# Kernel optimization log

Hardware: AMD Instinct MI355X
Metric: run time of the kernel (lower is better)

The kernel has to match this reference:

```python
import jax, jax.numpy as jnp
import numpy as np

N_CLIENTS = 1_000_000
N_ITEMS = 100_000
D = 128          # embedding_dim (in_feats)
H = 128          # output_size (h_feats)
N_NODES = 100_000
N_EDGES = 1_600_000


def setup_inputs() -> dict:
    key = jax.random.key(0)
    ks = jax.random.split(key, 12)
    f32 = jnp.float32
    return {
        # TwoPartEmbedding tables
        "client_table": jax.random.normal(ks[0], (N_CLIENTS, D), dtype=f32) * 0.02,
        "item_table": jax.random.normal(ks[1], (N_ITEMS, D), dtype=f32) * 0.02,
        # SAGEConv layer 1 (in_feats -> h_feats)
        "W_self1": jax.random.normal(ks[2], (D, H), dtype=f32) * (1.0 / np.sqrt(D)),
        "W_neigh1": jax.random.normal(ks[3], (D, H), dtype=f32) * (1.0 / np.sqrt(D)),
        "b1": jnp.zeros((H,), dtype=f32),
        # SAGEConv layer 2 (h_feats -> h_feats)
        "W_self2": jax.random.normal(ks[4], (H, H), dtype=f32) * (1.0 / np.sqrt(H)),
        "W_neigh2": jax.random.normal(ks[5], (H, H), dtype=f32) * (1.0 / np.sqrt(H)),
        "b2": jnp.zeros((H,), dtype=f32),
        # subgraph data
        "node_ids": jax.random.randint(ks[6], (N_NODES,), 0, N_CLIENTS + N_ITEMS),
        "src": jax.random.randint(ks[7], (N_EDGES,), 0, N_NODES),
        "dst": jax.random.randint(ks[8], (N_EDGES,), 0, N_NODES),
    }


def _two_part_embedding(node_ids, client_table, item_table):
    # IDs < N_CLIENTS index the client table; the rest (offset) index the item table.
    is_client = node_ids < N_CLIENTS
    cx = client_table[jnp.where(is_client, node_ids, 0)]              # [N, D]
    ix = item_table[jnp.where(is_client, 0, node_ids - N_CLIENTS)]    # [N, D]
    return jnp.where(is_client[:, None], cx, ix)


def _sage_layer(x, src, dst, W_self, W_neigh, b):
    # DGL SAGEConv, mean aggregator: gather src features, segment-mean onto dst.
    msg = x[src]  # [E, d]
    agg = jax.ops.segment_sum(msg, dst, num_segments=N_NODES)
    deg = jax.ops.segment_sum(jnp.ones((src.shape[0],), dtype=x.dtype), dst,
                              num_segments=N_NODES)
    h_neigh = agg / jnp.maximum(deg, 1.0)[:, None]
    return x @ W_self + h_neigh @ W_neigh + b


def reference(client_table, item_table, W_self1, W_neigh1, b1,
              W_self2, W_neigh2, b2, node_ids, src, dst):
    x = _two_part_embedding(node_ids, client_table, item_table)       # [N, D]
    h = jax.nn.relu(_sage_layer(x, src, dst, W_self1, W_neigh1, b1))  # [N, H]
    out = _sage_layer(h, src, dst, W_self2, W_neigh2, b2)             # [N, H]
    return out
```

## Files before the change

### kernel.cpp

```cpp
#include <hip/hip_runtime.h>


#define N_CLIENTS 1000000
#define N_NODES   100000
#define N_EDGES   1600000
#define DCAP      64

typedef unsigned short u16;
typedef unsigned int   u32;
typedef __bf16  bf16x8 __attribute__((ext_vector_type(8)));
typedef float   f32x4  __attribute__((ext_vector_type(4)));

__device__ __forceinline__ u16 f2bf(float f) {
    union { float f; u32 i; } c; c.f = f;
    u32 r = c.i + 0x7FFFu + ((c.i >> 16) & 1u);
    return (u16)(r >> 16);
}
__device__ __forceinline__ float2 bfpair(u32 u) {
    union { u32 i; float f; } lo, hi;
    lo.i = u << 16; hi.i = u & 0xFFFF0000u;
    return make_float2(lo.f, hi.f);
}

__global__ __launch_bounds__(256) void prep_kernel(
    const float* __restrict__ W0, const float* __restrict__ W1,
    const float* __restrict__ W2, const float* __restrict__ W3,
    u16* __restrict__ Wt)
{
    int i = blockIdx.x * 256 + threadIdx.x;
    int mat = i >> 14, k = (i >> 7) & 127, n = i & 127;
    const float* W = mat == 0 ? W0 : mat == 1 ? W1 : mat == 2 ? W2 : W3;
    Wt[mat * 16384 + n * 128 + k] = f2bf(W[k * 128 + n]);
}

__global__ __launch_bounds__(256) void embed_kernel(
    const float* __restrict__ client, const float* __restrict__ item,
    const int* __restrict__ ids, u16* __restrict__ Xb)
{
    int t = blockIdx.x * 256 + threadIdx.x;
    int node = t >> 5, j = t & 31;
    if (node >= N_NODES) return;
    int id = ids[node];
    const float4* row = (id < N_CLIENTS)
        ? (const float4*)(client + (size_t)id * 128)
        : (const float4*)(item + (size_t)(id - N_CLIENTS) * 128);
    float4 v = row[j];
    uint2 o;
    o.x = ((u32)f2bf(v.y) << 16) | f2bf(v.x);
    o.y = ((u32)f2bf(v.w) << 16) | f2bf(v.z);
    *(uint2*)(Xb + (size_t)node * 128 + j * 4) = o;
}

__global__ __launch_bounds__(256) void scatter_kernel(
    const int* __restrict__ src, const int* __restrict__ dst,
    int* __restrict__ cnt, int* __restrict__ bucket)
{
    int e = blockIdx.x * 256 + threadIdx.x;
    if (e >= N_EDGES) return;
    int d = dst[e];
    int pos = atomicAdd(&cnt[d], 1);
    if (pos < DCAP) bucket[(size_t)d * DCAP + pos] = src[e];
}

__global__ __launch_bounds__(256) void agg_kernel(
    const u16* __restrict__ Xb, const int* __restrict__ cnt,
    const int* __restrict__ bucket, u16* __restrict__ HNb)
{
    int wid = (blockIdx.x * 256 + threadIdx.x) >> 6;
    wid = __builtin_amdgcn_readfirstlane(wid);
    int lane = threadIdx.x & 63;
    if (wid >= N_NODES) return;
    int d = cnt[wid];
    int dc = d < DCAP ? d : DCAP;
    const int* bk = bucket + (size_t)wid * DCAP;
    float ax = 0.f, ay = 0.f;
    int e = 0;
    for (; e + 4 <= dc; e += 4) {
        int s0 = bk[e+0], s1 = bk[e+1], s2 = bk[e+2], s3 = bk[e+3];
        u32 u0 = *(const u32*)(Xb + (size_t)s0 * 128 + lane * 2);
        u32 u1 = *(const u32*)(Xb + (size_t)s1 * 128 + lane * 2);
        u32 u2 = *(const u32*)(Xb + (size_t)s2 * 128 + lane * 2);
        u32 u3 = *(const u32*)(Xb + (size_t)s3 * 128 + lane * 2);
        float2 v0 = bfpair(u0), v1 = bfpair(u1), v2 = bfpair(u2), v3 = bfpair(u3);
        ax += v0.x + v1.x + v2.x + v3.x;
        ay += v0.y + v1.y + v2.y + v3.y;
    }
    for (; e < dc; ++e) {
        float2 v = bfpair(*(const u32*)(Xb + (size_t)bk[e] * 128 + lane * 2));
        ax += v.x; ay += v.y;
    }
    float inv = 1.0f / fmaxf((float)d, 1.0f);
    *(u32*)(HNb + (size_t)wid * 128 + lane * 2) =
        ((u32)f2bf(ay * inv) << 16) | f2bf(ax * inv);
}

#define GB 64
__global__ __launch_bounds__(256) void gemm_kernel(
    const u16* __restrict__ Xb, const u16* __restrict__ HNb,
    const u16* __restrict__ Wts, const u16* __restrict__ Wtn,
    const float* __restrict__ bias,
    u16* __restrict__ OUTb, float* __restrict__ OUTf, int relu)
{
    __shared__ u16 wlds[128 * 144];
    int tid = threadIdx.x;
    int w = tid >> 6, lane = tid & 63;
    int m = lane & 15, q = lane >> 4;
    int r0 = blockIdx.x * GB;
    int rowa = r0 + w * 16 + m;
    int rowc = rowa < N_NODES ? rowa : N_NODES - 1;

    bf16x8 ax[4], ah[4];
    #pragma unroll
    for (int kc = 0; kc < 4; ++kc) {
        ax[kc] = *(const bf16x8*)(Xb  + (size_t)rowc * 128 + kc * 32 + q * 8);
        ah[kc] = *(const bf16x8*)(HNb + (size_t)rowc * 128 + kc * 32 + q * 8);
    }

    f32x4 acc[8];
    #pragma unroll
    for (int t = 0; t < 8; ++t) {
        float bv = bias[t * 16 + m];
        acc[t] = (f32x4){bv, bv, bv, bv};
    }

    for (int i = tid; i < 128 * 16; i += 256) {
        int n = i >> 4, c8 = i & 15;
        *(uint4*)&wlds[n * 144 + c8 * 8] = *(const uint4*)(Wts + n * 128 + c8 * 8);
    }
    __syncthreads();
    #pragma unroll
    for (int kc = 0; kc < 4; ++kc)
        #pragma unroll
        for (int t = 0; t < 8; ++t) {
            bf16x8 b = *(const bf16x8*)&wlds[(t * 16 + m) * 144 + kc * 32 + q * 8];
            acc[t] = __builtin_amdgcn_mfma_f32_16x16x32_bf16(ax[kc], b, acc[t], 0, 0, 0);
        }
    __syncthreads();

    for (int i = tid; i < 128 * 16; i += 256) {
        int n = i >> 4, c8 = i & 15;
        *(uint4*)&wlds[n * 144 + c8 * 8] = *(const uint4*)(Wtn + n * 128 + c8 * 8);
    }
    __syncthreads();
    #pragma unroll
    for (int kc = 0; kc < 4; ++kc)
        #pragma unroll
        for (int t = 0; t < 8; ++t) {
            bf16x8 b = *(const bf16x8*)&wlds[(t * 16 + m) * 144 + kc * 32 + q * 8];
            acc[t] = __builtin_amdgcn_mfma_f32_16x16x32_bf16(ah[kc], b, acc[t], 0, 0, 0);
        }

    #pragma unroll
    for (int t = 0; t < 8; ++t) {
        int col = t * 16 + m;
        #pragma unroll
        for (int r = 0; r < 4; ++r) {
            int row = r0 + w * 16 + q * 4 + r;
            if (row < N_NODES) {
                float v = acc[t][r];
                if (relu) v = fmaxf(v, 0.f);
                if (OUTb) OUTb[(size_t)row * 128 + col] = f2bf(v);
                else      OUTf[(size_t)row * 128 + col] = v;
            }
        }
    }
}

extern "C" void kernel_launch(void* const* d_in, const int* in_sizes, int n_in,
                              void* d_out, int out_size, void* d_ws, size_t ws_size,
                              hipStream_t stream) {
    const float* client = (const float*)d_in[0];
    const float* item   = (const float*)d_in[1];
    const float* Ws1    = (const float*)d_in[2];
    const float* Wn1    = (const float*)d_in[3];
    const float* b1     = (const float*)d_in[4];
    const float* Ws2    = (const float*)d_in[5];
    const float* Wn2    = (const float*)d_in[6];
    const float* b2     = (const float*)d_in[7];
    const int* node_ids = (const int*)d_in[8];
    const int* src      = (const int*)d_in[9];
    const int* dst      = (const int*)d_in[10];
    float* out = (float*)d_out;

    char* ws = (char*)d_ws;
    u16* xb     = (u16*)ws;
    u16* hnb    = (u16*)(ws + 25600000);
    int* cnt    = (int*)(ws + 51200000);
    int* bucket = (int*)(ws + 51600000);
    u16* Wt     = (u16*)(ws + 77200000);

    hipMemsetAsync(cnt, 0, N_NODES * sizeof(int), stream);
    prep_kernel   <<<256,   256, 0, stream>>>(Ws1, Wn1, Ws2, Wn2, Wt);
    embed_kernel  <<<12500, 256, 0, stream>>>(client, item, node_ids, xb);
    scatter_kernel<<<6250,  256, 0, stream>>>(src, dst, cnt, bucket);
    agg_kernel    <<<25000, 256, 0, stream>>>(xb, cnt, bucket, hnb);
    gemm_kernel   <<<1563,  256, 0, stream>>>(xb, hnb, Wt, Wt + 16384,
                                              b1, xb, (float*)nullptr, 1);
    agg_kernel    <<<25000, 256, 0, stream>>>(xb, cnt, bucket, hnb);
    gemm_kernel   <<<1563,  256, 0, stream>>>(xb, hnb, Wt + 32768, Wt + 49152,
                                              b2, (u16*)nullptr, out, 0);
}
```

Measured before the change: 1.025 ms.

## Fuse neighbor aggregation into GEMM kernel and merge front-end prep kernels

Merges the weight prep, embedding gather and edge bucketing kernels into one launch, with disjoint block ranges per task. Aggregation is fused into the layer GEMM: each wave computes the neighbor means for its 16 rows into shared memory, then runs the MFMA. This removes the HN round-trip through global memory and several launches. Layer 1 now writes to a separate buffer instead of in-place over xb, avoiding a read/write race. The cost is far fewer waves doing the latency-bound gather (1563 blocks with 16 serial rows per wave instead of 25000 blocks), which may hurt latency hiding.

```diff
diff --git a/kernel.cpp b/kernel.cpp
--- a/kernel.cpp
+++ b/kernel.cpp
@@ -22,86 +22,52 @@
     return make_float2(lo.f, hi.f);
 }
 
-__global__ __launch_bounds__(256) void prep_kernel(
+__global__ __launch_bounds__(256) void front_kernel(
+    const float* __restrict__ client, const float* __restrict__ item,
+    const int* __restrict__ ids,
+    const int* __restrict__ src, const int* __restrict__ dst,
     const float* __restrict__ W0, const float* __restrict__ W1,
     const float* __restrict__ W2, const float* __restrict__ W3,
+    u16* __restrict__ Xb, int* __restrict__ cnt, int* __restrict__ bucket,
     u16* __restrict__ Wt)
 {
-    int i = blockIdx.x * 256 + threadIdx.x;
-    int mat = i >> 14, k = (i >> 7) & 127, n = i & 127;
-    const float* W = mat == 0 ? W0 : mat == 1 ? W1 : mat == 2 ? W2 : W3;
-    Wt[mat * 16384 + n * 128 + k] = f2bf(W[k * 128 + n]);
-}
-
-__global__ __launch_bounds__(256) void embed_kernel(
-    const float* __restrict__ client, const float* __restrict__ item,
-    const int* __restrict__ ids, u16* __restrict__ Xb)
-{
-    int t = blockIdx.x * 256 + threadIdx.x;
-    int node = t >> 5, j = t & 31;
-    if (node >= N_NODES) return;
-    int id = ids[node];
-    const float4* row = (id < N_CLIENTS)
-        ? (const float4*)(client + (size_t)id * 128)
-        : (const float4*)(item + (size_t)(id - N_CLIENTS) * 128);
-    float4 v = row[j];
-    uint2 o;
-    o.x = ((u32)f2bf(v.y) << 16) | f2bf(v.x);
-    o.y = ((u32)f2bf(v.w) << 16) | f2bf(v.z);
-    *(uint2*)(Xb + (size_t)node * 128 + j * 4) = o;
-}
-
-__global__ __launch_bounds__(256) void scatter_kernel(
-    const int* __restrict__ src, const int* __restrict__ dst,
-    int* __restrict__ cnt, int* __restrict__ bucket)
-{
-    int e = blockIdx.x * 256 + threadIdx.x;
-    if (e >= N_EDGES) return;
-    int d = dst[e];
-    int pos = atomicAdd(&cnt[d], 1);
-    if (pos < DCAP) bucket[(size_t)d * DCAP + pos] = src[e];
-}
-
-__global__ __launch_bounds__(256) void agg_kernel(
-    const u16* __restrict__ Xb, const int* __restrict__ cnt,
-    const int* __restrict__ bucket, u16* __restrict__ HNb)
-{
-    int wid = (blockIdx.x * 256 + threadIdx.x) >> 6;
-    wid = __builtin_amdgcn_readfirstlane(wid);
-    int lane = threadIdx.x & 63;
-    if (wid >= N_NODES) return;
-    int d = cnt[wid];
-    int dc = d < DCAP ? d : DCAP;
-    const int* bk = bucket + (size_t)wid * DCAP;
-    float ax = 0.f, ay = 0.f;
-    int e = 0;
-    for (; e + 4 <= dc; e += 4) {
-        int s0 = bk[e+0], s1 = bk[e+1], s2 = bk[e+2], s3 = bk[e+3];
-        u32 u0 = *(const u32*)(Xb + (size_t)s0 * 128 + lane * 2);
-        u32 u1 = *(const u32*)(Xb + (size_t)s1 * 128 + lane * 2);
-        u32 u2 = *(const u32*)(Xb + (size_t)s2 * 128 + lane * 2);
-        u32 u3 = *(const u32*)(Xb + (size_t)s3 * 128 + lane * 2);
-        float2 v0 = bfpair(u0), v1 = bfpair(u1), v2 = bfpair(u2), v3 = bfpair(u3);
-        ax += v0.x + v1.x + v2.x + v3.x;
-        ay += v0.y + v1.y + v2.y + v3.y;
-    }
-    for (; e < dc; ++e) {
-        float2 v = bfpair(*(const u32*)(Xb + (size_t)bk[e] * 128 + lane * 2));
-        ax += v.x; ay += v.y;
-    }
-    float inv = 1.0f / fmaxf((float)d, 1.0f);
-    *(u32*)(HNb + (size_t)wid * 128 + lane * 2) =
-        ((u32)f2bf(ay * inv) << 16) | f2bf(ax * inv);
+    int b = blockIdx.x;
+    if (b < 6250) {
+        int e = b * 256 + threadIdx.x;
+        int d = dst[e];
+        int pos = atomicAdd(&cnt[d], 1);
+        if (pos < DCAP) bucket[(size_t)d * DCAP + pos] = src[e];
+    } else if (b < 18750) {
+        int t = (b - 6250) * 256 + threadIdx.x;
+        int node = t >> 5, j = t & 31;
+        if (node >= N_NODES) return;
+        int id = ids[node];
+        const float4* row = (id < N_CLIENTS)
+            ? (const float4*)(client + (size_t)id * 128)
+            : (const float4*)(item + (size_t)(id - N_CLIENTS) * 128);
+        float4 v = row[j];
+        uint2 o;
+        o.x = ((u32)f2bf(v.y) << 16) | f2bf(v.x);
+        o.y = ((u32)f2bf(v.w) << 16) | f2bf(v.z);
+        *(uint2*)(Xb + (size_t)node * 128 + j * 4) = o;
+    } else {
+        int i = (b - 18750) * 256 + threadIdx.x;
+        int mat = i >> 14, k = (i >> 7) & 127, n = i & 127;
+        const float* W = mat == 0 ? W0 : mat == 1 ? W1 : mat == 2 ? W2 : W3;
+        Wt[mat * 16384 + n * 128 + k] = f2bf(W[k * 128 + n]);
+    }
 }
 
 #define GB 64
-__global__ __launch_bounds__(256) void gemm_kernel(
-    const u16* __restrict__ Xb, const u16* __restrict__ HNb,
+__global__ __launch_bounds__(256) void layer_kernel(
+    const u16* __restrict__ Xin,
+    const int* __restrict__ cnt, const int* __restrict__ bucket,
     const u16* __restrict__ Wts, const u16* __restrict__ Wtn,
     const float* __restrict__ bias,
     u16* __restrict__ OUTb, float* __restrict__ OUTf, int relu)
 {
     __shared__ u16 wlds[128 * 144];
+    __shared__ u16 hnl[GB * 136];
     int tid = threadIdx.x;
     int w = tid >> 6, lane = tid & 63;
     int m = lane & 15, q = lane >> 4;
@@ -109,12 +75,52 @@
     int rowa = r0 + w * 16 + m;
     int rowc = rowa < N_NODES ? rowa : N_NODES - 1;
 
-    bf16x8 ax[4], ah[4];
-    #pragma unroll
-    for (int kc = 0; kc < 4; ++kc) {
-        ax[kc] = *(const bf16x8*)(Xb  + (size_t)rowc * 128 + kc * 32 + q * 8);
-        ah[kc] = *(const bf16x8*)(HNb + (size_t)rowc * 128 + kc * 32 + q * 8);
-    }
+    for (int i = tid; i < 128 * 16; i += 256) {
+        int n = i >> 4, c8 = i & 15;
+        *(uint4*)&wlds[n * 144 + c8 * 8] = *(const uint4*)(Wts + n * 128 + c8 * 8);
+    }
+
+    bf16x8 ax[4];
+    #pragma unroll
+    for (int kc = 0; kc < 4; ++kc)
+        ax[kc] = *(const bf16x8*)(Xin + (size_t)rowc * 128 + kc * 32 + q * 8);
+
+    for (int rr = 0; rr < 16; ++rr) {
+        int drow = r0 + w * 16 + rr;
+        int dv = drow < N_NODES ? drow : N_NODES - 1;
+        dv = __builtin_amdgcn_readfirstlane(dv);
+        int d = cnt[dv];
+        int dc = d < DCAP ? d : DCAP;
+        const int* bk = bucket + (size_t)dv * DCAP;
+        float sx = 0.f, sy = 0.f;
+        int e = 0;
+        for (; e + 8 <= dc; e += 8) {
+            u32 u[8];
+            #pragma unroll
+            for (int z = 0; z < 8; ++z) {
+                int s = bk[e + z];
+                u[z] = *(const u32*)(Xin + (size_t)s * 128 + lane * 2);
+            }
+            #pragma unroll
+            for (int z = 0; z < 8; ++z) {
+                float2 v = bfpair(u[z]);
+                sx += v.x; sy += v.y;
+            }
+        }
+        for (; e < dc; ++e) {
+            float2 v = bfpair(*(const u32*)(Xin + (size_t)bk[e] * 128 + lane * 2));
+            sx += v.x; sy += v.y;
+        }
+        float inv = 1.0f / fmaxf((float)d, 1.0f);
+        *(u32*)&hnl[(w * 16 + rr) * 136 + lane * 2] =
+            ((u32)f2bf(sy * inv) << 16) | f2bf(sx * inv);
+    }
+    __syncthreads();
+
+    bf16x8 ah[4];
+    #pragma unroll
+    for (int kc = 0; kc < 4; ++kc)
+        ah[kc] = *(const bf16x8*)&hnl[(w * 16 + m) * 136 + kc * 32 + q * 8];
 
     f32x4 acc[8];
     #pragma unroll
@@ -123,17 +129,12 @@
         acc[t] = (f32x4){bv, bv, bv, bv};
     }
 
-    for (int i = tid; i < 128 * 16; i += 256) {
-        int n = i >> 4, c8 = i & 15;
-        *(uint4*)&wlds[n * 144 + c8 * 8] = *(const uint4*)(Wts + n * 128 + c8 * 8);
-    }
-    __syncthreads();
     #pragma unroll
     for (int kc = 0; kc < 4; ++kc)
         #pragma unroll
         for (int t = 0; t < 8; ++t) {
-            bf16x8 b = *(const bf16x8*)&wlds[(t * 16 + m) * 144 + kc * 32 + q * 8];
-            acc[t] = __builtin_amdgcn_mfma_f32_16x16x32_bf16(ax[kc], b, acc[t], 0, 0, 0);
+            bf16x8 bfr = *(const bf16x8*)&wlds[(t * 16 + m) * 144 + kc * 32 + q * 8];
+            acc[t] = __builtin_amdgcn_mfma_f32_16x16x32_bf16(ax[kc], bfr, acc[t], 0, 0, 0);
         }
     __syncthreads();
 
@@ -146,8 +147,8 @@
     for (int kc = 0; kc < 4; ++kc)
         #pragma unroll
         for (int t = 0; t < 8; ++t) {
-            bf16x8 b = *(const bf16x8*)&wlds[(t * 16 + m) * 144 + kc * 32 + q * 8];
-            acc[t] = __builtin_amdgcn_mfma_f32_16x16x32_bf16(ah[kc], b, acc[t], 0, 0, 0);
+            bf16x8 bfr = *(const bf16x8*)&wlds[(t * 16 + m) * 144 + kc * 32 + q * 8];
+            acc[t] = __builtin_amdgcn_mfma_f32_16x16x32_bf16(ah[kc], bfr, acc[t], 0, 0, 0);
         }
 
     #pragma unroll
@@ -184,19 +185,17 @@
 
     char* ws = (char*)d_ws;
     u16* xb     = (u16*)ws;
-    u16* hnb    = (u16*)(ws + 25600000);
+    u16* hb     = (u16*)(ws + 25600000);
     int* cnt    = (int*)(ws + 51200000);
     int* bucket = (int*)(ws + 51600000);
     u16* Wt     = (u16*)(ws + 77200000);
 
     hipMemsetAsync(cnt, 0, N_NODES * sizeof(int), stream);
-    prep_kernel   <<<256,   256, 0, stream>>>(Ws1, Wn1, Ws2, Wn2, Wt);
-    embed_kernel  <<<12500, 256, 0, stream>>>(client, item, node_ids, xb);
-    scatter_kernel<<<6250,  256, 0, stream>>>(src, dst, cnt, bucket);
-    agg_kernel    <<<25000, 256, 0, stream>>>(xb, cnt, bucket, hnb);
-    gemm_kernel   <<<1563,  256, 0, stream>>>(xb, hnb, Wt, Wt + 16384,
-                                              b1, xb, (float*)nullptr, 1);
-    agg_kernel    <<<25000, 256, 0, stream>>>(xb, cnt, bucket, hnb);
-    gemm_kernel   <<<1563,  256, 0, stream>>>(xb, hnb, Wt + 32768, Wt + 49152,
-                                              b2, (u16*)nullptr, out, 0);
-}
+    front_kernel<<<19006, 256, 0, stream>>>(client, item, node_ids, src, dst,
+                                            Ws1, Wn1, Ws2, Wn2,
+                                            xb, cnt, bucket, Wt);
+    layer_kernel<<<1563, 256, 0, stream>>>(xb, cnt, bucket, Wt, Wt + 16384,
+                                           b1, hb, (float*)nullptr, 1);
+    layer_kernel<<<1563, 256, 0, stream>>>(hb, cnt, bucket, Wt + 32768, Wt + 49152,
+                                           b2, (u16*)nullptr, out, 0);
+}
```

After: 1.025 ms. No clear change (+0.0%).
